# Performance work log

Measured on AMD Instinct MI355X. Metric: run time of the kernel, lower is better.

The kernel has to match this reference:

```python
import jax, jax.numpy as jnp
import numpy as np

N, D = 100000, 128

def _seg_softmax(vals, ids, n):
    # torch scatter_reduce amax with include_self=True over zeros init => max(0, seg max);
    # softmax is shift-invariant so this matches torch exactly and stays stable.
    m = jnp.maximum(jax.ops.segment_max(vals, ids, num_segments=n), 0.0)
    e = jnp.exp(vals - m[ids])
    s = jax.ops.segment_sum(e, ids, num_segments=n)
    return e / (s[ids] + 1e-9)

def setup_inputs() -> dict:
    key = jax.random.key(0)
    ks = jax.random.split(key, 24)
    d = D
    def lin(k, fi, fo):
        b = 1.0 / np.sqrt(fi)
        kw, kb = jax.random.split(k)
        return (jax.random.uniform(kw, (fi, fo), jnp.float32, -b, b),
                jax.random.uniform(kb, (fo,), jnp.float32, -b, b))
    Wae, bae = lin(ks[0], 2 * d, d)
    w0w, w0b = lin(ks[1], d, 1)
    War, bar = lin(ks[2], 2 * d, d)
    w1w, w1b = lin(ks[3], d, 1)
    W1, b1 = lin(ks[4], d, d)
    W2, b2 = lin(ks[5], d, d)
    W3, b3 = lin(ks[6], d, d)
    return {
        'node_emb': jax.random.normal(ks[7], (N, d), jnp.float32),
        'Wae': Wae, 'bae': bae, 'w0w': w0w[:, 0], 'w0b': w0b,
        'War': War, 'bar': bar, 'w1w': w1w[:, 0], 'w1b': w1b,
        'W1': W1, 'b1': b1, 'W2': W2, 'b2': b2, 'W3': W3, 'b3': b3,
        'er_src': jax.random.randint(ks[8], (500000,), 0, N),
        'er_dst': jax.random.randint(ks[9], (500000,), 0, N),
        'ee_src': jax.random.randint(ks[10], (500000,), 0, N),
        'ee_dst': jax.random.randint(ks[11], (500000,), 0, N),
        'rr_src': jax.random.randint(ks[12], (200000,), 0, N),
        'rr_dst': jax.random.randint(ks[13], (200000,), 0, N),
    }

def reference(node_emb, Wae, bae, w0w, w0b, War, bar, w1w, w1b,
              W1, b1, W2, b2, W3, b3,
              er_src, er_dst, ee_src, ee_dst, rr_src, rr_dst):
    n = node_emb.shape[0]
    h = node_emb[er_src]              # (E, d) head entity emb
    r = node_emb[er_dst]              # (E, d) relation emb
    # entity-side attention over relation neighbours
    pair_e = jnp.concatenate([r, h], axis=-1)
    e_ij = jnp.tanh(pair_e @ Wae + bae) @ w0w + w0b[0]
    attn_e = _seg_softmax(e_ij, er_src, n)
    attn_agg = jax.ops.segment_sum(attn_e[:, None] * r, er_src, num_segments=n)
    # relation-side attention over entity neighbours (separate params)
    pair_r = jnp.concatenate([h, r], axis=-1)
    e_ij_r = jnp.tanh(pair_r @ War + bar) @ w1w + w1b[0]
    attn_r = _seg_softmax(e_ij_r, er_dst, n)
    attn_agg = attn_agg + jax.ops.segment_sum(attn_r[:, None] * h, er_dst, num_segments=n)
    # unweighted mean over similar-entity and similar-relation edges
    mean_agg = jax.ops.segment_sum(node_emb[ee_dst], ee_src, num_segments=n)
    mean_agg = mean_agg + jax.ops.segment_sum(node_emb[rr_dst], rr_src, num_segments=n)
    cnt = jax.ops.segment_sum(jnp.ones(ee_src.shape[0], node_emb.dtype), ee_src, num_segments=n)
    cnt = cnt + jax.ops.segment_sum(jnp.ones(rr_src.shape[0], node_emb.dtype), rr_src, num_segments=n)
    mean_agg = mean_agg / jnp.maximum(cnt, 1.0)[:, None]
    return (jnp.tanh(node_emb @ W1 + b1)
            + jnp.tanh(attn_agg @ W2 + b2)
            + jnp.tanh(mean_agg @ W3 + b3))
```

## Files before the change

### kernel.cpp

```cpp
#include <hip/hip_runtime.h>
#include <hip/hip_bf16.h>

#define D 128
#define TILE 2048

typedef __bf16 bf16x8 __attribute__((ext_vector_type(8)));
typedef float f32x4 __attribute__((ext_vector_type(4)));
typedef unsigned short u16x8 __attribute__((ext_vector_type(8)));

__device__ __forceinline__ float tanh_fast(float x) {
    float e = __expf(2.0f * fabsf(x));
    float t = 1.0f - 2.0f * __builtin_amdgcn_rcpf(e + 1.0f);
    return copysignf(t, x);
}

__device__ __forceinline__ float bf2f(unsigned short u) {
    return __uint_as_float((unsigned int)u << 16);
}

__device__ __forceinline__ unsigned short f2bf_u16(float x) {
    __hip_bfloat16 t = __float2bfloat16(x);
    return *(unsigned short*)&t;
}

#define SWZ_F(x, imm) __int_as_float(__builtin_amdgcn_ds_swizzle(__float_as_int(x), imm))

__global__ __launch_bounds__(256) void detect_kernel(const unsigned short* __restrict__ x,
                                                     int* __restrict__ flag) {
    int t = threadIdx.x;
    int cnt = 0;
    for (int i = t; i < 4096; i += 256) {
        unsigned e = (x[i] >> 7) & 0xFFu;
        if (e == 0xFFu || e >= 0x90u || (e >= 1u && e <= 0x6Eu)) cnt++;
    }
    __shared__ int sh[256];
    sh[t] = cnt;
    __syncthreads();
    for (int off = 128; off; off >>= 1) {
        if (t < off) sh[t] += sh[t + off];
        __syncthreads();
    }
    if (t == 0) flag[0] = (sh[0] > 800) ? 1 : 0;
}

struct ConvBatch {
    const void* src[14];
    __hip_bfloat16* dst[14];
    int n[14];
};

__global__ __launch_bounds__(256) void conv_weights_kernel(ConvBatch cb,
                                                           const int* __restrict__ flag) {
    int a = blockIdx.y;
    const void* s = cb.src[a];
    unsigned short* d = (unsigned short*)cb.dst[a];
    int n = cb.n[a];
    int f = flag[0];
    int i = (blockIdx.x * 256 + threadIdx.x) * 4;
    if (i >= n) return;
    if (i + 4 <= n) {
        ushort4 o;
        if (f) {
            float4 v = *(const float4*)((const float*)s + i);
            o.x = f2bf_u16(v.x); o.y = f2bf_u16(v.y);
            o.z = f2bf_u16(v.z); o.w = f2bf_u16(v.w);
        } else {
            o = *(const ushort4*)((const unsigned short*)s + i);
        }
        *(ushort4*)(d + i) = o;
    } else {
        for (int j = i; j < n; j++)
            d[j] = f ? f2bf_u16(((const float*)s)[j])
                     : ((const unsigned short*)s)[j];
    }
}

__global__ __launch_bounds__(256) void conv_x_kernel(const void* __restrict__ src,
                                                     __hip_bfloat16* __restrict__ dst,
                                                     int n, const int* __restrict__ flag) {
    int i = (blockIdx.x * 256 + threadIdx.x) * 4;
    if (i >= n) return;
    int f = flag[0];
    ushort4 o;
    if (f) {
        float4 v = *(const float4*)((const float*)src + i);
        o.x = f2bf_u16(v.x); o.y = f2bf_u16(v.y);
        o.z = f2bf_u16(v.z); o.w = f2bf_u16(v.w);
    } else {
        o = *(const ushort4*)((const unsigned short*)src + i);
    }
    *(ushort4*)((unsigned short*)dst + i) = o;
}

struct TransBatch {
    const void* base[7];
    int off[7];
    unsigned short* dst[7];
};

__global__ __launch_bounds__(256) void trans_kernel(TransBatch tb,
                                                    const int* __restrict__ flag) {
    int a = blockIdx.y;
    int f = flag[0];
    const float* sf = (const float*)tb.base[a] + tb.off[a];
    const unsigned short* sb = (const unsigned short*)tb.base[a] + tb.off[a];
    unsigned short* d = tb.dst[a];
    int idx = (blockIdx.x * 256 + threadIdx.x) * 4;
    int k = idx >> 7, c = idx & 127;
    unsigned short v[4];
    if (f) {
        float4 x = *(const float4*)(sf + idx);
        v[0] = f2bf_u16(x.x); v[1] = f2bf_u16(x.y);
        v[2] = f2bf_u16(x.z); v[3] = f2bf_u16(x.w);
    } else {
        ushort4 x = *(const ushort4*)(sb + idx);
        v[0] = x.x; v[1] = x.y; v[2] = x.z; v[3] = x.w;
    }
#pragma unroll
    for (int j = 0; j < 4; j++) d[(c + j) * 128 + k] = v[j];
}

__global__ __launch_bounds__(256) void zero_kernel(int* p, int n) {
    int i = blockIdx.x * 256 + threadIdx.x;
    if (i < n) p[i] = 0;
}

__global__ __launch_bounds__(256) void count4_kernel(const int* __restrict__ k0,
                                                     const int* __restrict__ k1,
                                                     const int* __restrict__ k2,
                                                     const int* __restrict__ k3,
                                                     int E0, int E1, int E2, int E3,
                                                     int* __restrict__ deg, int N) {
    int y = blockIdx.y;
    const int* k = (y == 0) ? k0 : (y == 1) ? k1 : (y == 2) ? k2 : k3;
    int E = (y == 0) ? E0 : (y == 1) ? E1 : (y == 2) ? E2 : E3;
    int i = blockIdx.x * 256 + threadIdx.x;
    if (i < E) atomicAdd(&deg[y * N + k[i]], 1);
}

__global__ __launch_bounds__(256) void scan_partial_kernel(const int* __restrict__ deg,
                                                           int* __restrict__ tsum,
                                                           int N, int ntpa) {
    int a = blockIdx.x / ntpa, t = blockIdx.x % ntpa;
    const int* d = deg + (size_t)a * N + (size_t)t * TILE;
    int lim = N - t * TILE; if (lim > TILE) lim = TILE;
    int base = threadIdx.x * 8;
    int s = 0;
#pragma unroll
    for (int j = 0; j < 8; j++) {
        int i = base + j;
        if (i < lim) s += d[i];
    }
    __shared__ int sh[256];
    sh[threadIdx.x] = s;
    __syncthreads();
    for (int off = 128; off; off >>= 1) {
        if (threadIdx.x < off) sh[threadIdx.x] += sh[threadIdx.x + off];
        __syncthreads();
    }
    if (threadIdx.x == 0) tsum[blockIdx.x] = sh[0];
}

__global__ __launch_bounds__(256) void scan_tiles_kernel(const int* __restrict__ tsum,
                                                         int* __restrict__ toff,
                                                         int* __restrict__ indptr,
                                                         int N, int ntpa) {
    __shared__ int tmp[256];
    int t = threadIdx.x;
    for (int a = 0; a < 4; a++) {
        int v = (t < ntpa) ? tsum[a * ntpa + t] : 0;
        tmp[t] = v;
        __syncthreads();
        for (int off = 1; off < 256; off <<= 1) {
            int u = (t >= off) ? tmp[t - off] : 0;
            __syncthreads();
            tmp[t] += u;
            __syncthreads();
        }
        if (t < ntpa) toff[a * ntpa + t] = tmp[t] - v;
        if (t == ntpa - 1) indptr[(size_t)a * (N + 1) + N] = tmp[t];
        __syncthreads();
    }
}

__global__ __launch_bounds__(256) void scan_final_kernel(int* __restrict__ degcur,
                                                         const int* __restrict__ toff,
                                                         int* __restrict__ indptr,
                                                         int N, int ntpa) {
    int a = blockIdx.x / ntpa, t = blockIdx.x % ntpa;
    int* d = degcur + (size_t)a * N + (size_t)t * TILE;
    int* ip = indptr + (size_t)a * (N + 1) + (size_t)t * TILE;
    int lim = N - t * TILE; if (lim > TILE) lim = TILE;
    int base = threadIdx.x * 8;
    int v[8];
    int s = 0;
#pragma unroll
    for (int j = 0; j < 8; j++) {
        int i = base + j;
        v[j] = (i < lim) ? d[i] : 0;
        s += v[j];
    }
    __shared__ int tmp[256];
    tmp[threadIdx.x] = s;
    __syncthreads();
    for (int off = 1; off < 256; off <<= 1) {
        int u = (threadIdx.x >= off) ? tmp[threadIdx.x - off] : 0;
        __syncthreads();
        tmp[threadIdx.x] += u;
        __syncthreads();
    }
    int run = toff[blockIdx.x] + tmp[threadIdx.x] - s;
#pragma unroll
    for (int j = 0; j < 8; j++) {
        int i = base + j;
        if (i < lim) { ip[i] = run; d[i] = run; run += v[j]; }
    }
}

__global__ __launch_bounds__(256) void scatter_attn2_kernel(const int* __restrict__ er_src,
                                                            const int* __restrict__ er_dst, int E,
                                                            int* __restrict__ cursor, int N,
                                                            int2* __restrict__ koth_e,
                                                            int2* __restrict__ koth_r) {
    int y = blockIdx.y;
    int i = blockIdx.x * 256 + threadIdx.x;
    if (i >= E) return;
    const int* keys = y ? er_dst : er_src;
    const int* oths = y ? er_src : er_dst;
    int* cur = cursor + (size_t)y * N;
    int2* ko = y ? koth_r : koth_e;
    int k = keys[i];
    int p = atomicAdd(&cur[k], 1);
    ko[p] = make_int2(k, oths[i]);
}

__global__ __launch_bounds__(256) void scatter_mean2_kernel(const int* __restrict__ ee_src,
                                                            const int* __restrict__ ee_dst, int Eee,
                                                            const int* __restrict__ rr_src,
                                                            const int* __restrict__ rr_dst, int Err,
                                                            int* __restrict__ cursor, int N,
                                                            int* __restrict__ dst_ee,
                                                            int* __restrict__ dst_rr) {
    int y = blockIdx.y;
    const int* keys = y ? rr_src : ee_src;
    const int* dsts = y ? rr_dst : ee_dst;
    int E = y ? Err : Eee;
    int* cur = cursor + (size_t)(2 + y) * N;
    int* ds = y ? dst_rr : dst_ee;
    int i = blockIdx.x * 256 + threadIdx.x;
    if (i < E) {
        int p = atomicAdd(&cur[keys[i]], 1);
        ds[p] = dsts[i];
    }
}

__global__ __launch_bounds__(256) void gemm2_mfma_kernel(
    const __hip_bfloat16* __restrict__ X,
    const unsigned short* __restrict__ Wt,
    const __hip_bfloat16* __restrict__ bias,
    __hip_bfloat16* __restrict__ part0,
    __hip_bfloat16* __restrict__ part1, int N) {
    __shared__ __align__(16) unsigned short Bs[128 * 136];
    int n0 = blockIdx.x * 64;
    int w = threadIdx.x >> 6, lane = threadIdx.x & 63;
    int n15 = lane & 15, quad = lane >> 4;
    int arow = n0 + w * 16 + n15;
    const unsigned short* ap = (const unsigned short*)X + (size_t)arow * D + quad * 8;
    bf16x8 af[4];
#pragma unroll
    for (int t = 0; t < 4; t++) {
        bf16x8 v = {};
        if (arow < N) v = *(const bf16x8*)(ap + t * 32);
        af[t] = v;
    }
    for (int half = 0; half < 2; half++) {
        if (half) __syncthreads();
        for (int idx = threadIdx.x; idx < 128 * 16; idx += 256) {
            int r = idx >> 4, ch = idx & 15;
            uint4 v = ((const uint4*)(Wt + (size_t)(half * 128 + r) * D))[ch];
            *(uint4*)&Bs[r * 136 + ch * 8] = v;
        }
        __syncthreads();
        __hip_bfloat16* outp = half ? part1 : part0;
        for (int c = 0; c < 8; c++) {
            f32x4 acc = {0.f, 0.f, 0.f, 0.f};
            const unsigned short* brow = &Bs[(c * 16 + n15) * 136 + quad * 8];
#pragma unroll
            for (int t = 0; t < 4; t++)
                acc = __builtin_amdgcn_mfma_f32_16x16x32_bf16(
                    af[t], *(const bf16x8*)(brow + t * 32), acc, 0, 0, 0);
            int col = c * 16 + n15;
            float b = half ? __bfloat162float(bias[col]) : 0.f;
#pragma unroll
            for (int i = 0; i < 4; i++) {
                int row = n0 + w * 16 + quad * 4 + i;
                if (row < N) outp[(size_t)row * D + col] = __float2bfloat16(acc[i] + b);
            }
        }
    }
}

__global__ __launch_bounds__(256) void final_mfma_kernel(
    const __hip_bfloat16* __restrict__ X, const __hip_bfloat16* __restrict__ Agg,
    const __hip_bfloat16* __restrict__ Mn,
    const unsigned short* __restrict__ Wt1, const __hip_bfloat16* __restrict__ b1,
    const unsigned short* __restrict__ Wt2, const __hip_bfloat16* __restrict__ b2,
    const unsigned short* __restrict__ Wt3, const __hip_bfloat16* __restrict__ b3,
    void* __restrict__ out, const int* __restrict__ flag, int N) {
    __shared__ __align__(16) unsigned short As[64 * 136];
    __shared__ __align__(16) unsigned short Bs[128 * 136];
    int n0 = blockIdx.x * 64;
    int w = threadIdx.x >> 6, lane = threadIdx.x & 63;
    int n15 = lane & 15, quad = lane >> 4;
    float osum[8][4];
#pragma unroll
    for (int c = 0; c < 8; c++)
#pragma unroll
        for (int i = 0; i < 4; i++) osum[c][i] = 0.f;
    const __hip_bfloat16* srcs[3] = {X, Agg, Mn};
    const unsigned short* Wts[3] = {Wt1, Wt2, Wt3};
    const __hip_bfloat16* bs[3] = {b1, b2, b3};
    for (int m = 0; m < 3; m++) {
        if (m > 0) __syncthreads();
        const __hip_bfloat16* S = srcs[m];
        const unsigned short* Wm = Wts[m];
        for (int idx = threadIdx.x; idx < 64 * 16; idx += 256) {
            int r = idx >> 4, ch = idx & 15;
            uint4 v = make_uint4(0u, 0u, 0u, 0u);
            int n = n0 + r;
            if (n < N) v = ((const uint4*)(S + (size_t)n * D))[ch];
            *(uint4*)&As[r * 136 + ch * 8] = v;
        }
        for (int idx = threadIdx.x; idx < 128 * 16; idx += 256) {
            int r = idx >> 4, ch = idx & 15;
            uint4 v = ((const uint4*)(Wm + (size_t)r * D))[ch];
            *(uint4*)&Bs[r * 136 + ch * 8] = v;
        }
        __syncthreads();
        const unsigned short* arow = &As[(w * 16 + n15) * 136 + quad * 8];
        bf16x8 af[4];
#pragma unroll
        for (int t = 0; t < 4; t++) af[t] = *(const bf16x8*)(arow + t * 32);
        for (int c = 0; c < 8; c++) {
            f32x4 acc = {0.f, 0.f, 0.f, 0.f};
            const unsigned short* brow = &Bs[(c * 16 + n15) * 136 + quad * 8];
#pragma unroll
            for (int t = 0; t < 4; t++)
                acc = __builtin_amdgcn_mfma_f32_16x16x32_bf16(
                    af[t], *(const bf16x8*)(brow + t * 32), acc, 0, 0, 0);
            float bb = __bfloat162float(bs[m][c * 16 + n15]);
#pragma unroll
            for (int i = 0; i < 4; i++) osum[c][i] += tanh_fast(acc[i] + bb);
        }
    }
    int f = flag[0];
    for (int c = 0; c < 8; c++) {
        int col = c * 16 + n15;
#pragma unroll
        for (int i = 0; i < 4; i++) {
            int row = n0 + w * 16 + quad * 4 + i;
            if (row < N) {
                if (f) ((float*)out)[(size_t)row * D + col] = osum[c][i];
                else   ((__hip_bfloat16*)out)[(size_t)row * D + col] =
                           __float2bfloat16(osum[c][i]);
            }
        }
    }
}

__global__ __launch_bounds__(256) void edge_score_kernel(
    const __hip_bfloat16* __restrict__ Pkey,
    const __hip_bfloat16* __restrict__ Poth,
    const int2* __restrict__ koth,
    const __hip_bfloat16* __restrict__ w,
    const __hip_bfloat16* __restrict__ wb,
    float* __restrict__ eij, int E) {
    int l = threadIdx.x & 15;
    int gid = (int)((blockIdx.x * 256 + threadIdx.x) >> 4);
    int ngroups = (int)((gridDim.x * 256) >> 4);
    u16x8 wv = *(const u16x8*)((const unsigned short*)w + l * 8);
    float wf[8];
#pragma unroll
    for (int j = 0; j < 8; j++) wf[j] = bf2f(wv[j]);
    float wbv = bf2f(*(const unsigned short*)wb);
    const unsigned short* PK = (const unsigned short*)Pkey;
    const unsigned short* PO = (const unsigned short*)Poth;
    for (int s = gid; s < E; s += ngroups) {
        int2 ko = koth[s];
        u16x8 a = *(const u16x8*)(PK + (size_t)ko.x * D + l * 8);
        u16x8 b = *(const u16x8*)(PO + (size_t)ko.y * D + l * 8);
        float p = 0.f;
#pragma unroll
        for (int j = 0; j < 8; j++)
            p = fmaf(tanh_fast(bf2f(a[j]) + bf2f(b[j])), wf[j], p);
        p += SWZ_F(p, 0x041F);
        p += SWZ_F(p, 0x081F);
        p += SWZ_F(p, 0x101F);
        p += SWZ_F(p, 0x201F);
        if (l == 0) eij[s] = p + wbv;
    }
}

__global__ __launch_bounds__(256) void node_agg_kernel(
    const __hip_bfloat16* __restrict__ X,
    const float* __restrict__ eij_e, const int* __restrict__ ip_e,
    const int2* __restrict__ koth_e,
    const float* __restrict__ eij_r, const int* __restrict__ ip_r,
    const int2* __restrict__ koth_r,
    const int* __restrict__ ip_ee, const int* __restrict__ dst_ee,
    const int* __restrict__ ip_rr, const int* __restrict__ dst_rr,
    __hip_bfloat16* __restrict__ attn_agg,
    __hip_bfloat16* __restrict__ mean_agg, int N) {
    int g = (int)((blockIdx.x * 256 + threadIdx.x) >> 4);
    int l = threadIdx.x & 15;
    if (g >= N) return;
    const unsigned short* Xp = (const unsigned short*)X;
    float acc[8];
#pragma unroll
    for (int j = 0; j < 8; j++) acc[j] = 0.f;
    if (blockIdx.y == 0) {
        for (int side = 0; side < 2; side++) {
            const float* eij = side ? eij_r : eij_e;
            const int* ip  = side ? ip_r  : ip_e;
            const int2* ko = side ? koth_r : koth_e;
            int s0 = ip[g], s1 = ip[g + 1];
            if (s1 == s0) continue;
            float m = 0.f;
            for (int i = s0 + l; i < s1; i += 16) m = fmaxf(m, eij[i]);
            m = fmaxf(m, SWZ_F(m, 0x041F));
            m = fmaxf(m, SWZ_F(m, 0x081F));
            m = fmaxf(m, SWZ_F(m, 0x101F));
            m = fmaxf(m, SWZ_F(m, 0x201F));
            float ssum = 0.f;
            for (int i = s0 + l; i < s1; i += 16) ssum += __expf(eij[i] - m);
            ssum += SWZ_F(ssum, 0x041F);
            ssum += SWZ_F(ssum, 0x081F);
            ssum += SWZ_F(ssum, 0x101F);
            ssum += SWZ_F(ssum, 0x201F);
            float inv = 1.f / (ssum + 1e-9f);
            int i = s0;
            for (; i + 4 <= s1; i += 4) {
                int o0 = ko[i].y, o1 = ko[i + 1].y, o2 = ko[i + 2].y, o3 = ko[i + 3].y;
                u16x8 x0 = *(const u16x8*)(Xp + (size_t)o0 * D + l * 8);
                u16x8 x1 = *(const u16x8*)(Xp + (size_t)o1 * D + l * 8);
                u16x8 x2 = *(const u16x8*)(Xp + (size_t)o2 * D + l * 8);
                u16x8 x3 = *(const u16x8*)(Xp + (size_t)o3 * D + l * 8);
                float p0 = __expf(eij[i] - m) * inv;
                float p1 = __expf(eij[i + 1] - m) * inv;
                float p2 = __expf(eij[i + 2] - m) * inv;
                float p3 = __expf(eij[i + 3] - m) * inv;
#pragma unroll
                for (int j = 0; j < 8; j++)
                    acc[j] += p0 * bf2f(x0[j]) + p1 * bf2f(x1[j])
                            + p2 * bf2f(x2[j]) + p3 * bf2f(x3[j]);
            }
            for (; i < s1; i++) {
                int o0 = ko[i].y;
                u16x8 x0 = *(const u16x8*)(Xp + (size_t)o0 * D + l * 8);
                float p0 = __expf(eij[i] - m) * inv;
#pragma unroll
                for (int j = 0; j < 8; j++) acc[j] += p0 * bf2f(x0[j]);
            }
        }
        u16x8 ov;
#pragma unroll
        for (int j = 0; j < 8; j++) ov[j] = f2bf_u16(acc[j]);
        *(u16x8*)((unsigned short*)attn_agg + (size_t)g * D + l * 8) = ov;
    } else {
        int cnt = 0;
        for (int side = 0; side < 2; side++) {
            const int* ip  = side ? ip_rr  : ip_ee;
            const int* dst = side ? dst_rr : dst_ee;
            int s0 = ip[g], s1 = ip[g + 1];
            cnt += s1 - s0;
            int i = s0;
            for (; i + 4 <= s1; i += 4) {
                int o0 = dst[i], o1 = dst[i + 1], o2 = dst[i + 2], o3 = dst[i + 3];
                u16x8 x0 = *(const u16x8*)(Xp + (size_t)o0 * D + l * 8);
                u16x8 x1 = *(const u16x8*)(Xp + (size_t)o1 * D + l * 8);
                u16x8 x2 = *(const u16x8*)(Xp + (size_t)o2 * D + l * 8);
                u16x8 x3 = *(const u16x8*)(Xp + (size_t)o3 * D + l * 8);
#pragma unroll
                for (int j = 0; j < 8; j++)
                    acc[j] += (bf2f(x0[j]) + bf2f(x1[j]))
                            + (bf2f(x2[j]) + bf2f(x3[j]));
            }
            for (; i < s1; i++) {
                u16x8 x0 = *(const u16x8*)(Xp + (size_t)dst[i] * D + l * 8);
#pragma unroll
                for (int j = 0; j < 8; j++) acc[j] += bf2f(x0[j]);
            }
        }
        float inv = 1.f / fmaxf((float)cnt, 1.f);
        u16x8 ov;
#pragma unroll
        for (int j = 0; j < 8; j++) ov[j] = f2bf_u16(acc[j] * inv);
        *(u16x8*)((unsigned short*)mean_agg + (size_t)g * D + l * 8) = ov;
    }
}

extern "C" void kernel_launch(void* const* d_in, const int* in_sizes, int n_in,
                              void* d_out, int out_size, void* d_ws, size_t ws_size,
                              hipStream_t stream) {
    const int* er_src = (const int*)d_in[15];
    const int* er_dst = (const int*)d_in[16];
    const int* ee_src = (const int*)d_in[17];
    const int* ee_dst = (const int*)d_in[18];
    const int* rr_src = (const int*)d_in[19];
    const int* rr_dst = (const int*)d_in[20];

    int N   = in_sizes[0] / D;
    int Eer = in_sizes[15];
    int Eee = in_sizes[17];
    int Err = in_sizes[19];

    char* ws = (char*)d_ws;
    size_t off = 0;
    auto alloc = [&](size_t bytes) -> void* {
        void* p = ws + off;
        off = (off + bytes + 255) & ~(size_t)255;
        return p;
    };
    int ntpa = (N + TILE - 1) / TILE;
    int T = 4 * ntpa;
    int* flag   = (int*)alloc(256);
    int2* koth_e = (int2*)alloc((size_t)Eer * 8);
    int2* koth_r = (int2*)alloc((size_t)Eer * 8);
    int* dst_ee = (int*)alloc((size_t)Eee * 4);
    int* dst_rr = (int*)alloc((size_t)Err * 4);
    int* indptr = (int*)alloc((size_t)4 * (N + 1) * 4);
    int* degcur = (int*)alloc((size_t)4 * N * 4);
    int* tsum   = (int*)alloc((size_t)T * 4);
    int* toff   = (int*)alloc((size_t)T * 4);
    float* eij_e = (float*)alloc((size_t)Eer * 4);
    float* eij_r = (float*)alloc((size_t)Eer * 4);
    __hip_bfloat16* Xc = (__hip_bfloat16*)alloc((size_t)N * D * 2);
    __hip_bfloat16* part0 = (__hip_bfloat16*)alloc((size_t)N * D * 2);
    __hip_bfloat16* part1 = (__hip_bfloat16*)alloc((size_t)N * D * 2);
    __hip_bfloat16* attn_agg = part0;
    __hip_bfloat16* mean_agg = part1;
    unsigned short* WtA = (unsigned short*)alloc((size_t)256 * 128 * 2);
    unsigned short* WtR = (unsigned short*)alloc((size_t)256 * 128 * 2);
    unsigned short* Wt1 = (unsigned short*)alloc((size_t)128 * 128 * 2);
    unsigned short* Wt2 = (unsigned short*)alloc((size_t)128 * 128 * 2);
    unsigned short* Wt3 = (unsigned short*)alloc((size_t)128 * 128 * 2);
    ConvBatch cb;
    int widx[14] = {1, 2, 3, 4, 5, 6, 7, 8, 9, 10, 11, 12, 13, 14};
    for (int i = 0; i < 14; i++) {
        cb.src[i] = d_in[widx[i]];
        cb.n[i] = in_sizes[widx[i]];
        cb.dst[i] = (__hip_bfloat16*)alloc((size_t)cb.n[i] * 2);
    }
    const __hip_bfloat16* bae = cb.dst[1];
    const __hip_bfloat16* w0w = cb.dst[2];
    const __hip_bfloat16* w0b = cb.dst[3];
    const __hip_bfloat16* bar_= cb.dst[5];
    const __hip_bfloat16* w1w = cb.dst[6];
    const __hip_bfloat16* w1b = cb.dst[7];
    const __hip_bfloat16* b1  = cb.dst[9];
    const __hip_bfloat16* b2  = cb.dst[11];
    const __hip_bfloat16* b3  = cb.dst[13];
    (void)n_in; (void)out_size;
    if (off > ws_size) return;

    detect_kernel<<<1, 256, 0, stream>>>((const unsigned short*)d_in[0], flag);
    conv_weights_kernel<<<dim3(32, 14), 256, 0, stream>>>(cb, flag);
    conv_x_kernel<<<(N * D / 4 + 255) / 256, 256, 0, stream>>>(d_in[0], Xc, N * D, flag);
    TransBatch tb;
    tb.base[0] = d_in[1];  tb.off[0] = 0;         tb.dst[0] = WtA;
    tb.base[1] = d_in[1];  tb.off[1] = 128 * 128; tb.dst[1] = WtA + 128 * 128;
    tb.base[2] = d_in[5];  tb.off[2] = 0;         tb.dst[2] = WtR;
    tb.base[3] = d_in[5];  tb.off[3] = 128 * 128; tb.dst[3] = WtR + 128 * 128;
    tb.base[4] = d_in[9];  tb.off[4] = 0;         tb.dst[4] = Wt1;
    tb.base[5] = d_in[11]; tb.off[5] = 0;         tb.dst[5] = Wt2;
    tb.base[6] = d_in[13]; tb.off[6] = 0;         tb.dst[6] = Wt3;
    trans_kernel<<<dim3(16, 7), 256, 0, stream>>>(tb, flag);

    zero_kernel<<<(4 * N + 255) / 256, 256, 0, stream>>>(degcur, 4 * N);
    int Emax = Eer > Eee ? Eer : Eee;
    if (Err > Emax) Emax = Err;
    count4_kernel<<<dim3((Emax + 255) / 256, 4), 256, 0, stream>>>(
        er_src, er_dst, ee_src, rr_src, Eer, Eer, Eee, Err, degcur, N);
    scan_partial_kernel<<<T, 256, 0, stream>>>(degcur, tsum, N, ntpa);
    scan_tiles_kernel<<<1, 256, 0, stream>>>(tsum, toff, indptr, N, ntpa);
    scan_final_kernel<<<T, 256, 0, stream>>>(degcur, toff, indptr, N, ntpa);
    scatter_attn2_kernel<<<dim3((Eer + 255) / 256, 2), 256, 0, stream>>>(
        er_src, er_dst, Eer, degcur, N, koth_e, koth_r);
    int Emm = Eee > Err ? Eee : Err;
    scatter_mean2_kernel<<<dim3((Emm + 255) / 256, 2), 256, 0, stream>>>(
        ee_src, ee_dst, Eee, rr_src, rr_dst, Err, degcur, N, dst_ee, dst_rr);

    int GB = (N + 63) / 64;
    int EB = 2048;

    gemm2_mfma_kernel<<<GB, 256, 0, stream>>>(Xc, WtA, bae, part0, part1, N);
    edge_score_kernel<<<EB, 256, 0, stream>>>(part1, part0, koth_e,
                                              w0w, w0b, eij_e, Eer);

    gemm2_mfma_kernel<<<GB, 256, 0, stream>>>(Xc, WtR, bar_, part0, part1, N);
    edge_score_kernel<<<EB, 256, 0, stream>>>(part1, part0, koth_r,
                                              w1w, w1b, eij_r, Eer);

    int NG = (N + 15) / 16;
    node_agg_kernel<<<dim3(NG, 2), 256, 0, stream>>>(
        Xc, eij_e, indptr, koth_e, eij_r, indptr + (N + 1), koth_r,
        indptr + 2 * (N + 1), dst_ee, indptr + 3 * (N + 1), dst_rr,
        attn_agg, mean_agg, N);
    final_mfma_kernel<<<GB, 256, 0, stream>>>(Xc, attn_agg, mean_agg,
                                              Wt1, b1, Wt2, b2, Wt3, b3,
                                              d_out, flag, N);
}
```

Baseline: 553.1 us.

## Compute edge scores per key node via CSR and merge scatter kernels

Edge scoring now assigns one 16-lane group to each key node and walks its CSR segment. The key-side projection row is loaded once and reused for every edge of that node, instead of being gathered per edge through a stored (key, other) pair. The sorted edge lists therefore store only the other-endpoint index, which halves that array. The two scatter kernels are merged into a single four-way launch. The cost is possible load imbalance from skewed node degrees and a grid sized by node count rather than a fixed persistent grid.

```diff
diff --git a/kernel.cpp b/kernel.cpp
--- a/kernel.cpp
+++ b/kernel.cpp
@@ -217,40 +217,25 @@
     }
 }
 
-__global__ __launch_bounds__(256) void scatter_attn2_kernel(const int* __restrict__ er_src,
-                                                            const int* __restrict__ er_dst, int E,
-                                                            int* __restrict__ cursor, int N,
-                                                            int2* __restrict__ koth_e,
-                                                            int2* __restrict__ koth_r) {
+__global__ __launch_bounds__(256) void scatter4_kernel(
+    const int* __restrict__ k0, const int* __restrict__ p0,
+    const int* __restrict__ k1, const int* __restrict__ p1,
+    const int* __restrict__ k2, const int* __restrict__ p2,
+    const int* __restrict__ k3, const int* __restrict__ p3,
+    int E0, int E1, int E2, int E3,
+    int* __restrict__ cursor, int N,
+    int* __restrict__ o0, int* __restrict__ o1,
+    int* __restrict__ o2, int* __restrict__ o3) {
     int y = blockIdx.y;
-    int i = blockIdx.x * 256 + threadIdx.x;
-    if (i >= E) return;
-    const int* keys = y ? er_dst : er_src;
-    const int* oths = y ? er_src : er_dst;
+    const int* keys = (y == 0) ? k0 : (y == 1) ? k1 : (y == 2) ? k2 : k3;
+    const int* pays = (y == 0) ? p0 : (y == 1) ? p1 : (y == 2) ? p2 : p3;
+    int E = (y == 0) ? E0 : (y == 1) ? E1 : (y == 2) ? E2 : E3;
     int* cur = cursor + (size_t)y * N;
-    int2* ko = y ? koth_r : koth_e;
-    int k = keys[i];
-    int p = atomicAdd(&cur[k], 1);
-    ko[p] = make_int2(k, oths[i]);
-}
-
-__global__ __launch_bounds__(256) void scatter_mean2_kernel(const int* __restrict__ ee_src,
-                                                            const int* __restrict__ ee_dst, int Eee,
-                                                            const int* __restrict__ rr_src,
-                                                            const int* __restrict__ rr_dst, int Err,
-                                                            int* __restrict__ cursor, int N,
-                                                            int* __restrict__ dst_ee,
-                                                            int* __restrict__ dst_rr) {
-    int y = blockIdx.y;
-    const int* keys = y ? rr_src : ee_src;
-    const int* dsts = y ? rr_dst : ee_dst;
-    int E = y ? Err : Eee;
-    int* cur = cursor + (size_t)(2 + y) * N;
-    int* ds = y ? dst_rr : dst_ee;
+    int* out = (y == 0) ? o0 : (y == 1) ? o1 : (y == 2) ? o2 : o3;
     int i = blockIdx.x * 256 + threadIdx.x;
     if (i < E) {
         int p = atomicAdd(&cur[keys[i]], 1);
-        ds[p] = dsts[i];
+        out[p] = pays[i];
     }
 }
 
@@ -371,13 +356,16 @@
 __global__ __launch_bounds__(256) void edge_score_kernel(
     const __hip_bfloat16* __restrict__ Pkey,
     const __hip_bfloat16* __restrict__ Poth,
-    const int2* __restrict__ koth,
+    const int* __restrict__ ip,
+    const int* __restrict__ oth,
     const __hip_bfloat16* __restrict__ w,
     const __hip_bfloat16* __restrict__ wb,
-    float* __restrict__ eij, int E) {
+    float* __restrict__ eij, int N) {
+    int g = (int)((blockIdx.x * 256 + threadIdx.x) >> 4);
     int l = threadIdx.x & 15;
-    int gid = (int)((blockIdx.x * 256 + threadIdx.x) >> 4);
-    int ngroups = (int)((gridDim.x * 256) >> 4);
+    if (g >= N) return;
+    int s0 = ip[g], s1 = ip[g + 1];
+    if (s1 == s0) return;
     u16x8 wv = *(const u16x8*)((const unsigned short*)w + l * 8);
     float wf[8];
 #pragma unroll
@@ -385,28 +373,48 @@
     float wbv = bf2f(*(const unsigned short*)wb);
     const unsigned short* PK = (const unsigned short*)Pkey;
     const unsigned short* PO = (const unsigned short*)Poth;
-    for (int s = gid; s < E; s += ngroups) {
-        int2 ko = koth[s];
-        u16x8 a = *(const u16x8*)(PK + (size_t)ko.x * D + l * 8);
-        u16x8 b = *(const u16x8*)(PO + (size_t)ko.y * D + l * 8);
-        float p = 0.f;
+    u16x8 a = *(const u16x8*)(PK + (size_t)g * D + l * 8);
+    float av[8];
+#pragma unroll
+    for (int j = 0; j < 8; j++) av[j] = bf2f(a[j]);
+    int i = s0;
+    for (; i + 2 <= s1; i += 2) {
+        int o0 = oth[i], o1 = oth[i + 1];
+        u16x8 b0 = *(const u16x8*)(PO + (size_t)o0 * D + l * 8);
+        u16x8 b1 = *(const u16x8*)(PO + (size_t)o1 * D + l * 8);
+        float p0 = 0.f, p1 = 0.f;
+#pragma unroll
+        for (int j = 0; j < 8; j++) {
+            p0 = fmaf(tanh_fast(av[j] + bf2f(b0[j])), wf[j], p0);
+            p1 = fmaf(tanh_fast(av[j] + bf2f(b1[j])), wf[j], p1);
+        }
+        p0 += SWZ_F(p0, 0x041F); p1 += SWZ_F(p1, 0x041F);
+        p0 += SWZ_F(p0, 0x081F); p1 += SWZ_F(p1, 0x081F);
+        p0 += SWZ_F(p0, 0x101F); p1 += SWZ_F(p1, 0x101F);
+        p0 += SWZ_F(p0, 0x201F); p1 += SWZ_F(p1, 0x201F);
+        if (l == 0) { eij[i] = p0 + wbv; eij[i + 1] = p1 + wbv; }
+    }
+    if (i < s1) {
+        int o0 = oth[i];
+        u16x8 b0 = *(const u16x8*)(PO + (size_t)o0 * D + l * 8);
+        float p0 = 0.f;
 #pragma unroll
         for (int j = 0; j < 8; j++)
-            p = fmaf(tanh_fast(bf2f(a[j]) + bf2f(b[j])), wf[j], p);
-        p += SWZ_F(p, 0x041F);
-        p += SWZ_F(p, 0x081F);
-        p += SWZ_F(p, 0x101F);
-        p += SWZ_F(p, 0x201F);
-        if (l == 0) eij[s] = p + wbv;
+            p0 = fmaf(tanh_fast(av[j] + bf2f(b0[j])), wf[j], p0);
+        p0 += SWZ_F(p0, 0x041F);
+        p0 += SWZ_F(p0, 0x081F);
+        p0 += SWZ_F(p0, 0x101F);
+        p0 += SWZ_F(p0, 0x201F);
+        if (l == 0) eij[i] = p0 + wbv;
     }
 }
 
 __global__ __launch_bounds__(256) void node_agg_kernel(
     const __hip_bfloat16* __restrict__ X,
     const float* __restrict__ eij_e, const int* __restrict__ ip_e,
-    const int2* __restrict__ koth_e,
+    const int* __restrict__ oth_e,
     const float* __restrict__ eij_r, const int* __restrict__ ip_r,
-    const int2* __restrict__ koth_r,
+    const int* __restrict__ oth_r,
     const int* __restrict__ ip_ee, const int* __restrict__ dst_ee,
     const int* __restrict__ ip_rr, const int* __restrict__ dst_rr,
     __hip_bfloat16* __restrict__ attn_agg,
@@ -422,7 +430,7 @@
         for (int side = 0; side < 2; side++) {
             const float* eij = side ? eij_r : eij_e;
             const int* ip  = side ? ip_r  : ip_e;
-            const int2* ko = side ? koth_r : koth_e;
+            const int* oth = side ? oth_r : oth_e;
             int s0 = ip[g], s1 = ip[g + 1];
             if (s1 == s0) continue;
             float m = 0.f;
@@ -440,7 +448,7 @@
             float inv = 1.f / (ssum + 1e-9f);
             int i = s0;
             for (; i + 4 <= s1; i += 4) {
-                int o0 = ko[i].y, o1 = ko[i + 1].y, o2 = ko[i + 2].y, o3 = ko[i + 3].y;
+                int o0 = oth[i], o1 = oth[i + 1], o2 = oth[i + 2], o3 = oth[i + 3];
                 u16x8 x0 = *(const u16x8*)(Xp + (size_t)o0 * D + l * 8);
                 u16x8 x1 = *(const u16x8*)(Xp + (size_t)o1 * D + l * 8);
                 u16x8 x2 = *(const u16x8*)(Xp + (size_t)o2 * D + l * 8);
@@ -455,7 +463,7 @@
                             + p2 * bf2f(x2[j]) + p3 * bf2f(x3[j]);
             }
             for (; i < s1; i++) {
-                int o0 = ko[i].y;
+                int o0 = oth[i];
                 u16x8 x0 = *(const u16x8*)(Xp + (size_t)o0 * D + l * 8);
                 float p0 = __expf(eij[i] - m) * inv;
 #pragma unroll
@@ -524,8 +532,8 @@
     int ntpa = (N + TILE - 1) / TILE;
     int T = 4 * ntpa;
     int* flag   = (int*)alloc(256);
-    int2* koth_e = (int2*)alloc((size_t)Eer * 8);
-    int2* koth_r = (int2*)alloc((size_t)Eer * 8);
+    int* oth_e  = (int*)alloc((size_t)Eer * 4);
+    int* oth_r  = (int*)alloc((size_t)Eer * 4);
     int* dst_ee = (int*)alloc((size_t)Eee * 4);
     int* dst_rr = (int*)alloc((size_t)Err * 4);
     int* indptr = (int*)alloc((size_t)4 * (N + 1) * 4);
@@ -584,26 +592,23 @@
     scan_partial_kernel<<<T, 256, 0, stream>>>(degcur, tsum, N, ntpa);
     scan_tiles_kernel<<<1, 256, 0, stream>>>(tsum, toff, indptr, N, ntpa);
     scan_final_kernel<<<T, 256, 0, stream>>>(degcur, toff, indptr, N, ntpa);
-    scatter_attn2_kernel<<<dim3((Eer + 255) / 256, 2), 256, 0, stream>>>(
-        er_src, er_dst, Eer, degcur, N, koth_e, koth_r);
-    int Emm = Eee > Err ? Eee : Err;
-    scatter_mean2_kernel<<<dim3((Emm + 255) / 256, 2), 256, 0, stream>>>(
-        ee_src, ee_dst, Eee, rr_src, rr_dst, Err, degcur, N, dst_ee, dst_rr);
+    scatter4_kernel<<<dim3((Emax + 255) / 256, 4), 256, 0, stream>>>(
+        er_src, er_dst, er_dst, er_src, ee_src, ee_dst, rr_src, rr_dst,
+        Eer, Eer, Eee, Err, degcur, N, oth_e, oth_r, dst_ee, dst_rr);
 
     int GB = (N + 63) / 64;
-    int EB = 2048;
+    int NG = (N + 15) / 16;
 
     gemm2_mfma_kernel<<<GB, 256, 0, stream>>>(Xc, WtA, bae, part0, part1, N);
-    edge_score_kernel<<<EB, 256, 0, stream>>>(part1, part0, koth_e,
-                                              w0w, w0b, eij_e, Eer);
+    edge_score_kernel<<<NG, 256, 0, stream>>>(part1, part0, indptr, oth_e,
+                                              w0w, w0b, eij_e, N);
 
     gemm2_mfma_kernel<<<GB, 256, 0, stream>>>(Xc, WtR, bar_, part0, part1, N);
-    edge_score_kernel<<<EB, 256, 0, stream>>>(part1, part0, koth_r,
-                                              w1w, w1b, eij_r, Eer);
-
-    int NG = (N + 15) / 16;
+    edge_score_kernel<<<NG, 256, 0, stream>>>(part1, part0, indptr + (N + 1), oth_r,
+                                              w1w, w1b, eij_r, N);
+
     node_agg_kernel<<<dim3(NG, 2), 256, 0, stream>>>(
-        Xc, eij_e, indptr, koth_e, eij_r, indptr + (N + 1), koth_r,
+        Xc, eij_e, indptr, oth_e, eij_r, indptr + (N + 1), oth_r,
         indptr + 2 * (N + 1), dst_ee, indptr + 3 * (N + 1), dst_rr,
         attn_agg, mean_agg, N);
     final_mfma_kernel<<<GB, 256, 0, stream>>>(Xc, attn_agg, mean_agg,
```

Measured after the change: 586.1 us. 1.06x slower.
